# Kernel optimization log

Measured on AMD Instinct MI355X. Metric: run time of the kernel, lower is better.

Reference implementation:

```python
import jax, jax.numpy as jnp
import numpy as np

NUM_ITERS = 5
NUM_SPATIAL = 3          # S: xyz spatial dims
THETA_ALPHA = 1.0
THETA_BETA = 1.0
THETA_GAMMA = 8.0


def _gauss_filter(f, q):
    """Exact Gaussian filtering (math the permutohedral lattice pl.apply approximates).
    f: [D, N] features, q: [C, N] values.
    out[:, i] = sum_j exp(-0.5 * ||f_i - f_j||^2) * q[:, j]
    """
    f2 = jnp.sum(f * f, axis=0)                       # [N]
    d2 = f2[:, None] + f2[None, :] - 2.0 * (f.T @ f)  # [N, N] squared distances
    K = jnp.exp(-0.5 * d2)                            # symmetric Gaussian kernel
    return q @ K                                      # [C, N]


def setup_inputs() -> dict:
    key = jax.random.key(0)
    k1, k2 = jax.random.split(key)
    C, N, D = 10, 8192, 6
    unaries = jax.random.normal(k1, (C, N), dtype=jnp.float32)
    feat = jax.random.normal(k2, (D, N), dtype=jnp.float32)
    # learned params: diagonal init for filter weights, Potts (-I) compatibility
    spatial_weights = jnp.eye(C, dtype=jnp.float32)
    bilateral_weights = jnp.eye(C, dtype=jnp.float32)
    compatibility_matrix = -jnp.eye(C, dtype=jnp.float32)
    return {
        "unaries": unaries,
        "feat": feat,
        "spatial_weights": spatial_weights,
        "bilateral_weights": bilateral_weights,
        "compatibility_matrix": compatibility_matrix,
    }


def reference(unaries, feat, spatial_weights, bilateral_weights, compatibility_matrix):
    # Pre-scaled features (torch code scales per-iteration, but with
    # theta_alpha=theta_beta=1.0 the in-place aliasing division is a no-op).
    sp_feat = feat[:NUM_SPATIAL] / THETA_GAMMA                      # [S, N]
    bl_feat = jnp.concatenate(
        [feat[:NUM_SPATIAL] / THETA_ALPHA, feat[NUM_SPATIAL:] / THETA_BETA],
        axis=0,
    )                                                               # [S+F, N]

    q = unaries
    for _ in range(NUM_ITERS):
        p = jax.nn.softmax(q, axis=0)                               # over classes
        spatial_out = _gauss_filter(sp_feat, p)                     # [C, N]
        bilateral_out = _gauss_filter(bl_feat, p)                   # [C, N]
        message_passing = spatial_weights @ spatial_out + bilateral_weights @ bilateral_out
        pairwise = compatibility_matrix @ message_passing
        q = unaries - pairwise
    return q
```

## Files before the change

kernel.cpp:

```cpp
#include <hip/hip_runtime.h>
#include <math.h>

#define N 8192
#define C 10
#define NUM_ITERS 5
#define FBLOCK 1024
#define IBLK 32
#define NBLK (N / IBLK)
#define JW (N / 16)
#define NS (JW / 32)
#define LOG2E 1.44269504088896340736f
#define C3 (LOG2E / 64.0f)

typedef _Float16 half8 __attribute__((ext_vector_type(8)));
typedef _Float16 half4 __attribute__((ext_vector_type(4)));
typedef _Float16 half2 __attribute__((ext_vector_type(2)));
typedef float f32x4 __attribute__((ext_vector_type(4)));

#define WS_AJS 0
#define WS_AJB (N * 16)
#define WS_PF0 (N * 32)
#define WS_PF1 (N * 64)
#define PFIDX(n, c) ((((n) >> 4) * 16 + (c)) * 16 + ((n) & 15))

static __device__ __forceinline__ half4 expcvt(f32x4 d) {
    float e0 = __builtin_amdgcn_exp2f(d[0]);
    float e1 = __builtin_amdgcn_exp2f(d[1]);
    float e2 = __builtin_amdgcn_exp2f(d[2]);
    float e3 = __builtin_amdgcn_exp2f(d[3]);
    half2 lo = __builtin_bit_cast(half2, __builtin_amdgcn_cvt_pkrtz(e0, e1));
    half2 hi = __builtin_bit_cast(half2, __builtin_amdgcn_cvt_pkrtz(e2, e3));
    half4 r = {lo[0], lo[1], hi[0], hi[1]};
    return r;
}

#define GROUP(AF, PF_, B1A, B1B, ACCA, ACCB)                                         \
    {                                                                                \
        f32x4 _da = __builtin_amdgcn_mfma_f32_16x16x16f16(AF, B1A, zero, 0, 0, 0);   \
        f32x4 _db = __builtin_amdgcn_mfma_f32_16x16x16f16(AF, B1B, zero, 0, 0, 0);   \
        half4 _wa = expcvt(_da), _wb = expcvt(_db);                                  \
        ACCA = __builtin_amdgcn_mfma_f32_16x16x16f16(_wa, PF_, ACCA, 0, 0, 0);       \
        ACCB = __builtin_amdgcn_mfma_f32_16x16x16f16(_wb, PF_, ACCB, 0, 0, 0);       \
    }

__global__ __launch_bounds__(256) void init_kernel(
    const float* __restrict__ unaries, const float* __restrict__ feat,
    half8* __restrict__ ajs8, half8* __restrict__ ajb8,
    _Float16* __restrict__ pf0, _Float16* __restrict__ pf1) {
    int n = blockIdx.x * 256 + threadIdx.x;
    float f6[6];
#pragma unroll
    for (int d = 0; d < 6; ++d) f6[d] = feat[d * N + n];
    float h3 = 0.5f * (f6[0] * f6[0] + f6[1] * f6[1] + f6[2] * f6[2]);
    float h6v = h3 + 0.5f * (f6[3] * f6[3] + f6[4] * f6[4] + f6[5] * f6[5]);
    half8 a = {};
    a[0] = (_Float16)(f6[0] * C3);
    a[1] = (_Float16)(f6[1] * C3);
    a[2] = (_Float16)(f6[2] * C3);
    a[6] = (_Float16)(-h3 * C3);
    a[7] = (_Float16)1.0f;
    ajs8[n] = a;
    half8 b;
#pragma unroll
    for (int d = 0; d < 6; ++d) b[d] = (_Float16)(f6[d] * LOG2E);
    b[6] = (_Float16)(-h6v * LOG2E);
    b[7] = (_Float16)1.0f;
    ajb8[n] = b;

    float q[C];
#pragma unroll
    for (int c = 0; c < C; ++c) q[c] = unaries[c * N + n];
    float m = q[0];
#pragma unroll
    for (int c = 1; c < C; ++c) m = fmaxf(m, q[c]);
    float e[C], s = 0.0f;
#pragma unroll
    for (int c = 0; c < C; ++c) {
        e[c] = __builtin_amdgcn_exp2f((q[c] - m) * LOG2E);
        s += e[c];
    }
    float inv = 1.0f / s;
#pragma unroll
    for (int c = 0; c < C; ++c) pf0[PFIDX(n, c)] = (_Float16)(e[c] * inv);
#pragma unroll
    for (int c = C; c < 16; ++c) {
        pf0[PFIDX(n, c)] = (_Float16)0.0f;
        pf1[PFIDX(n, c)] = (_Float16)0.0f;
    }
}

__global__ __launch_bounds__(FBLOCK, 4) void fused_kernel(
    const float* __restrict__ unaries, const float* __restrict__ feat,
    const float* __restrict__ SW, const float* __restrict__ BW,
    const float* __restrict__ CM,
    const half4* __restrict__ ajs_g, const half4* __restrict__ ajb_g,
    const _Float16* __restrict__ pf_in, _Float16* __restrict__ pf_out,
    float* __restrict__ out, int is_last) {
    __shared__ float rbuf[16 * 1024];
    int t = threadIdx.x;
    int i0 = blockIdx.x * IBLK;
    int lane = t & 63;
    int w = t >> 6;
    int il = lane & 15;
    int quad = lane >> 4;
    int h = quad & 1;
    bool klo = (quad < 2);
    const half4 hz = {};
    const f32x4 zero = {0.f, 0.f, 0.f, 0.f};

    half4 b1s0, b1s1, b1b0, b1b1;
#pragma unroll
    for (int s = 0; s < 2; ++s) {
        int i = i0 + s * 16 + il;
        float g0 = feat[0 * N + i], g1 = feat[1 * N + i], g2 = feat[2 * N + i];
        float g3 = feat[3 * N + i], g4 = feat[4 * N + i], g5 = feat[5 * N + i];
        float h3 = 0.5f * (g0 * g0 + g1 * g1 + g2 * g2);
        float h6v = h3 + 0.5f * (g3 * g3 + g4 * g4 + g5 * g5);
        half4 slo = {(_Float16)g0, (_Float16)g1, (_Float16)g2, (_Float16)0.0f};
        half4 shi = {(_Float16)0.0f, (_Float16)0.0f, (_Float16)1.0f, (_Float16)(-h3 * C3)};
        half4 blo = {(_Float16)g0, (_Float16)g1, (_Float16)g2, (_Float16)g3};
        half4 bhi = {(_Float16)g4, (_Float16)g5, (_Float16)1.0f, (_Float16)(-h6v * LOG2E)};
        half4 vs = klo ? (h ? shi : slo) : hz;
        half4 vb = klo ? (h ? bhi : blo) : hz;
        if (s == 0) { b1s0 = vs; b1b0 = vb; } else { b1s1 = vs; b1b1 = vb; }
    }

    f32x4 as0 = zero, as1 = zero, ab0 = zero, ab1 = zero;

    int jw = w * JW;
    const half4* pfv = (const half4*)pf_in;

    half4 cvs0 = ajs_g[(jw + il) * 2 + h];
    half4 cvs1 = ajs_g[(jw + 16 + il) * 2 + h];
    half4 cvb0 = ajb_g[(jw + il) * 2 + h];
    half4 cvb1 = ajb_g[(jw + 16 + il) * 2 + h];
    half4 cp0 = pfv[((jw >> 4) * 16 + il) * 4 + quad];
    half4 cp1 = pfv[((jw >> 4) * 16 + 16 + il) * 4 + quad];

#pragma unroll 4
    for (int k = 0; k < NS; ++k) {
        int jn = jw + (((k + 1) & (NS - 1)) * 32);
        half4 nvs0 = ajs_g[(jn + il) * 2 + h];
        half4 nvs1 = ajs_g[(jn + 16 + il) * 2 + h];
        half4 nvb0 = ajb_g[(jn + il) * 2 + h];
        half4 nvb1 = ajb_g[(jn + 16 + il) * 2 + h];
        half4 np0 = pfv[((jn >> 4) * 16 + il) * 4 + quad];
        half4 np1 = pfv[((jn >> 4) * 16 + 16 + il) * 4 + quad];

        GROUP(cvs0, cp0, b1s0, b1s1, as0, as1);
        GROUP(cvs1, cp1, b1s0, b1s1, as0, as1);
        GROUP(cvb0, cp0, b1b0, b1b1, ab0, ab1);
        GROUP(cvb1, cp1, b1b0, b1b1, ab0, ab1);

        cvs0 = nvs0; cvs1 = nvs1; cvb0 = nvb0; cvb1 = nvb1;
        cp0 = np0; cp1 = np1;
    }

    {
        float* rb = rbuf + w * 1024;
#pragma unroll
        for (int r = 0; r < 4; ++r) {
            rb[r * 64 + lane]       = as0[r];
            rb[256 + r * 64 + lane] = as1[r];
            rb[512 + r * 64 + lane] = ab0[r];
            rb[768 + r * 64 + lane] = ab1[r];
        }
    }
    __syncthreads();
    {
        float tot = 0.f;
#pragma unroll
        for (int w2 = 0; w2 < 16; ++w2) tot += rbuf[w2 * 1024 + t];
        rbuf[t] = tot;
    }
    __syncthreads();

    if (t < IBLK) {
        int i = i0 + t;
        int sub = t >> 4, ql = (t & 15) >> 2, rr = t & 3;
        float sp[C], bl[C];
#pragma unroll
        for (int c = 0; c < C; ++c) {
            int base = sub * 256 + rr * 64 + ql * 16 + c;
            sp[c] = rbuf[base];
            bl[c] = rbuf[base + 512];
        }
        float msg[C];
#pragma unroll
        for (int c = 0; c < C; ++c) {
            float m = 0.f;
#pragma unroll
            for (int k = 0; k < C; ++k)
                m += SW[c * C + k] * sp[k] + BW[c * C + k] * bl[k];
            msg[c] = m;
        }
        float qq[C];
#pragma unroll
        for (int c = 0; c < C; ++c) {
            float pw = 0.f;
#pragma unroll
            for (int k = 0; k < C; ++k) pw += CM[c * C + k] * msg[k];
            qq[c] = unaries[c * N + i] - pw;
        }
        if (is_last) {
#pragma unroll
            for (int c = 0; c < C; ++c) out[c * N + i] = qq[c];
        } else {
            float m = qq[0];
#pragma unroll
            for (int c = 1; c < C; ++c) m = fmaxf(m, qq[c]);
            float e[C], s = 0.0f;
#pragma unroll
            for (int c = 0; c < C; ++c) {
                e[c] = __builtin_amdgcn_exp2f((qq[c] - m) * LOG2E);
                s += e[c];
            }
            float inv = 1.0f / s;
#pragma unroll
            for (int c = 0; c < C; ++c) pf_out[PFIDX(i, c)] = (_Float16)(e[c] * inv);
        }
    }
}

extern "C" void kernel_launch(void* const* d_in, const int* in_sizes, int n_in,
                              void* d_out, int out_size, void* d_ws, size_t ws_size,
                              hipStream_t stream) {
    const float* unaries = (const float*)d_in[0];
    const float* feat    = (const float*)d_in[1];
    const float* SW      = (const float*)d_in[2];
    const float* BW      = (const float*)d_in[3];
    const float* CM      = (const float*)d_in[4];
    float* out = (float*)d_out;

    char* ws = (char*)d_ws;
    half8* ajs    = (half8*)(ws + WS_AJS);
    half8* ajb    = (half8*)(ws + WS_AJB);
    _Float16* pf0 = (_Float16*)(ws + WS_PF0);
    _Float16* pf1 = (_Float16*)(ws + WS_PF1);

    init_kernel<<<N / 256, 256, 0, stream>>>(unaries, feat, ajs, ajb, pf0, pf1);
    const _Float16* pin = pf0;
    _Float16* pout = pf1;
    for (int it = 1; it <= NUM_ITERS; ++it) {
        fused_kernel<<<NBLK, FBLOCK, 0, stream>>>(
            unaries, feat, SW, BW, CM, (const half4*)ajs, (const half4*)ajb,
            pin, pout, out, it == NUM_ITERS ? 1 : 0);
        const _Float16* tmp = pout;
        pout = (_Float16*)pin;
        pin = tmp;
    }
}
```

Measured before the change: 167.2 us.

## Shrink row tile to 16 rows per block and drop software prefetch

Each block now computes 16 output rows instead of 32. That halves the per-wave accumulators and the per-block reduction buffer, and doubles the block count. The register-level double-buffered prefetch of the j-tile operands is removed and loads are issued inside the loop, with the occupancy hint raised from 4 to 8. The aim is more occupancy and a smaller LDS and register footprint. In exchange, each loaded A and P fragment is reused for one B column tile instead of two, which doubles global and L2 traffic per MFMA, and latency hiding now depends on occupancy rather than explicit prefetch.

After: 193.5 us. +15.7%, slower.

```diff
diff --git a/kernel.cpp b/kernel.cpp
--- a/kernel.cpp
+++ b/kernel.cpp
@@ -5,7 +5,7 @@
 #define C 10
 #define NUM_ITERS 5
 #define FBLOCK 1024
-#define IBLK 32
+#define IBLK 16
 #define NBLK (N / IBLK)
 #define JW (N / 16)
 #define NS (JW / 32)
@@ -34,13 +34,11 @@
     return r;
 }
 
-#define GROUP(AF, PF_, B1A, B1B, ACCA, ACCB)                                         \
+#define GROUP(AF, PF_, B1, ACC)                                                      \
     {                                                                                \
-        f32x4 _da = __builtin_amdgcn_mfma_f32_16x16x16f16(AF, B1A, zero, 0, 0, 0);   \
-        f32x4 _db = __builtin_amdgcn_mfma_f32_16x16x16f16(AF, B1B, zero, 0, 0, 0);   \
-        half4 _wa = expcvt(_da), _wb = expcvt(_db);                                  \
-        ACCA = __builtin_amdgcn_mfma_f32_16x16x16f16(_wa, PF_, ACCA, 0, 0, 0);       \
-        ACCB = __builtin_amdgcn_mfma_f32_16x16x16f16(_wb, PF_, ACCB, 0, 0, 0);       \
+        f32x4 _d = __builtin_amdgcn_mfma_f32_16x16x16f16(AF, B1, zero, 0, 0, 0);     \
+        half4 _w = expcvt(_d);                                                       \
+        ACC = __builtin_amdgcn_mfma_f32_16x16x16f16(_w, PF_, ACC, 0, 0, 0);          \
     }
 
 __global__ __launch_bounds__(256) void init_kernel(
@@ -89,14 +87,14 @@
     }
 }
 
-__global__ __launch_bounds__(FBLOCK, 4) void fused_kernel(
+__global__ __launch_bounds__(FBLOCK, 8) void fused_kernel(
     const float* __restrict__ unaries, const float* __restrict__ feat,
     const float* __restrict__ SW, const float* __restrict__ BW,
     const float* __restrict__ CM,
     const half4* __restrict__ ajs_g, const half4* __restrict__ ajb_g,
     const _Float16* __restrict__ pf_in, _Float16* __restrict__ pf_out,
     float* __restrict__ out, int is_last) {
-    __shared__ float rbuf[16 * 1024];
+    __shared__ float rbuf[16 * 512];
     int t = threadIdx.x;
     int i0 = blockIdx.x * IBLK;
     int lane = t & 63;
@@ -108,10 +106,9 @@
     const half4 hz = {};
     const f32x4 zero = {0.f, 0.f, 0.f, 0.f};
 
-    half4 b1s0, b1s1, b1b0, b1b1;
-#pragma unroll
-    for (int s = 0; s < 2; ++s) {
-        int i = i0 + s * 16 + il;
+    half4 b1s, b1b;
+    {
+        int i = i0 + il;
         float g0 = feat[0 * N + i], g1 = feat[1 * N + i], g2 = feat[2 * N + i];
         float g3 = feat[3 * N + i], g4 = feat[4 * N + i], g5 = feat[5 * N + i];
         float h3 = 0.5f * (g0 * g0 + g1 * g1 + g2 * g2);
@@ -120,78 +117,60 @@
         half4 shi = {(_Float16)0.0f, (_Float16)0.0f, (_Float16)1.0f, (_Float16)(-h3 * C3)};
         half4 blo = {(_Float16)g0, (_Float16)g1, (_Float16)g2, (_Float16)g3};
         half4 bhi = {(_Float16)g4, (_Float16)g5, (_Float16)1.0f, (_Float16)(-h6v * LOG2E)};
-        half4 vs = klo ? (h ? shi : slo) : hz;
-        half4 vb = klo ? (h ? bhi : blo) : hz;
-        if (s == 0) { b1s0 = vs; b1b0 = vb; } else { b1s1 = vs; b1b1 = vb; }
-    }
-
-    f32x4 as0 = zero, as1 = zero, ab0 = zero, ab1 = zero;
+        b1s = klo ? (h ? shi : slo) : hz;
+        b1b = klo ? (h ? bhi : blo) : hz;
+    }
+
+    f32x4 acc_s = zero, acc_b = zero;
 
     int jw = w * JW;
     const half4* pfv = (const half4*)pf_in;
 
-    half4 cvs0 = ajs_g[(jw + il) * 2 + h];
-    half4 cvs1 = ajs_g[(jw + 16 + il) * 2 + h];
-    half4 cvb0 = ajb_g[(jw + il) * 2 + h];
-    half4 cvb1 = ajb_g[(jw + 16 + il) * 2 + h];
-    half4 cp0 = pfv[((jw >> 4) * 16 + il) * 4 + quad];
-    half4 cp1 = pfv[((jw >> 4) * 16 + 16 + il) * 4 + quad];
-
-#pragma unroll 4
+#pragma unroll 2
     for (int k = 0; k < NS; ++k) {
-        int jn = jw + (((k + 1) & (NS - 1)) * 32);
-        half4 nvs0 = ajs_g[(jn + il) * 2 + h];
-        half4 nvs1 = ajs_g[(jn + 16 + il) * 2 + h];
-        half4 nvb0 = ajb_g[(jn + il) * 2 + h];
-        half4 nvb1 = ajb_g[(jn + 16 + il) * 2 + h];
-        half4 np0 = pfv[((jn >> 4) * 16 + il) * 4 + quad];
-        half4 np1 = pfv[((jn >> 4) * 16 + 16 + il) * 4 + quad];
-
-        GROUP(cvs0, cp0, b1s0, b1s1, as0, as1);
-        GROUP(cvs1, cp1, b1s0, b1s1, as0, as1);
-        GROUP(cvb0, cp0, b1b0, b1b1, ab0, ab1);
-        GROUP(cvb1, cp1, b1b0, b1b1, ab0, ab1);
-
-        cvs0 = nvs0; cvs1 = nvs1; cvb0 = nvb0; cvb1 = nvb1;
-        cp0 = np0; cp1 = np1;
+        int j0 = jw + k * 32;
+        half4 cvs0 = ajs_g[(j0 + il) * 2 + h];
+        half4 cvs1 = ajs_g[(j0 + 16 + il) * 2 + h];
+        half4 cvb0 = ajb_g[(j0 + il) * 2 + h];
+        half4 cvb1 = ajb_g[(j0 + 16 + il) * 2 + h];
+        half4 cp0 = pfv[((j0 >> 4) * 16 + il) * 4 + quad];
+        half4 cp1 = pfv[(((j0 >> 4) + 1) * 16 + il) * 4 + quad];
+
+        GROUP(cvs0, cp0, b1s, acc_s);
+        GROUP(cvs1, cp1, b1s, acc_s);
+        GROUP(cvb0, cp0, b1b, acc_b);
+        GROUP(cvb1, cp1, b1b, acc_b);
     }
 
     {
-        float* rb = rbuf + w * 1024;
+        float* rb = rbuf + w * 512;
 #pragma unroll
         for (int r = 0; r < 4; ++r) {
-            rb[r * 64 + lane]       = as0[r];
-            rb[256 + r * 64 + lane] = as1[r];
-            rb[512 + r * 64 + lane] = ab0[r];
-            rb[768 + r * 64 + lane] = ab1[r];
+            rb[r * 64 + lane]       = acc_s[r];
+            rb[256 + r * 64 + lane] = acc_b[r];
         }
     }
     __syncthreads();
-    {
+    if (t < 512) {
         float tot = 0.f;
 #pragma unroll
-        for (int w2 = 0; w2 < 16; ++w2) tot += rbuf[w2 * 1024 + t];
+        for (int w2 = 0; w2 < 16; ++w2) tot += rbuf[w2 * 512 + t];
         rbuf[t] = tot;
     }
     __syncthreads();
 
     if (t < IBLK) {
         int i = i0 + t;
-        int sub = t >> 4, ql = (t & 15) >> 2, rr = t & 3;
-        float sp[C], bl[C];
-#pragma unroll
-        for (int c = 0; c < C; ++c) {
-            int base = sub * 256 + rr * 64 + ql * 16 + c;
-            sp[c] = rbuf[base];
-            bl[c] = rbuf[base + 512];
-        }
+        int q16 = t >> 2, r = t & 3;
+        int base = r * 64 + q16 * 16;
         float msg[C];
 #pragma unroll
         for (int c = 0; c < C; ++c) {
             float m = 0.f;
 #pragma unroll
-            for (int k = 0; k < C; ++k)
-                m += SW[c * C + k] * sp[k] + BW[c * C + k] * bl[k];
+            for (int kk = 0; kk < C; ++kk)
+                m += SW[c * C + kk] * rbuf[base + kk] +
+                     BW[c * C + kk] * rbuf[256 + base + kk];
             msg[c] = m;
         }
         float qq[C];
@@ -199,7 +178,7 @@
         for (int c = 0; c < C; ++c) {
             float pw = 0.f;
 #pragma unroll
-            for (int k = 0; k < C; ++k) pw += CM[c * C + k] * msg[k];
+            for (int kk = 0; kk < C; ++kk) pw += CM[c * C + kk] * msg[kk];
             qq[c] = unaries[c * N + i] - pw;
         }
         if (is_last) {
```

## Software-pipeline distance MFMAs ahead of exp and accumulate MFMAs

Applied to the files above, without the earlier changes.

Restructures the inner j-loop into a two-stage software pipeline. The distance MFMAs for the next chunk are issued before the exp/convert and accumulation MFMAs of the current chunk, with double-buffered operand loads. This lets MFMA latency and transcendental VALU work overlap instead of each group waiting on its own distance result. It raises register pressure from holding eight f32x4 distance tiles plus two operand sets, and the fixed trip count of 7 hardcodes NS=16.

Result: no change. 166.1 us (-0.7%).

```diff
diff --git a/kernel.cpp b/kernel.cpp
--- a/kernel.cpp
+++ b/kernel.cpp
@@ -34,14 +34,8 @@
     return r;
 }
 
-#define GROUP(AF, PF_, B1A, B1B, ACCA, ACCB)                                         \
-    {                                                                                \
-        f32x4 _da = __builtin_amdgcn_mfma_f32_16x16x16f16(AF, B1A, zero, 0, 0, 0);   \
-        f32x4 _db = __builtin_amdgcn_mfma_f32_16x16x16f16(AF, B1B, zero, 0, 0, 0);   \
-        half4 _wa = expcvt(_da), _wb = expcvt(_db);                                  \
-        ACCA = __builtin_amdgcn_mfma_f32_16x16x16f16(_wa, PF_, ACCA, 0, 0, 0);       \
-        ACCB = __builtin_amdgcn_mfma_f32_16x16x16f16(_wb, PF_, ACCB, 0, 0, 0);       \
-    }
+struct Ops { half4 vs0, vs1, vb0, vb1, p0, p1; };
+struct Dset { f32x4 d0, d1, d2, d3, d4, d5, d6, d7; };
 
 __global__ __launch_bounds__(256) void init_kernel(
     const float* __restrict__ unaries, const float* __restrict__ feat,
@@ -126,35 +120,67 @@
     }
 
     f32x4 as0 = zero, as1 = zero, ab0 = zero, ab1 = zero;
-
     int jw = w * JW;
     const half4* pfv = (const half4*)pf_in;
 
-    half4 cvs0 = ajs_g[(jw + il) * 2 + h];
-    half4 cvs1 = ajs_g[(jw + 16 + il) * 2 + h];
-    half4 cvb0 = ajb_g[(jw + il) * 2 + h];
-    half4 cvb1 = ajb_g[(jw + 16 + il) * 2 + h];
-    half4 cp0 = pfv[((jw >> 4) * 16 + il) * 4 + quad];
-    half4 cp1 = pfv[((jw >> 4) * 16 + 16 + il) * 4 + quad];
-
-#pragma unroll 4
-    for (int k = 0; k < NS; ++k) {
-        int jn = jw + (((k + 1) & (NS - 1)) * 32);
-        half4 nvs0 = ajs_g[(jn + il) * 2 + h];
-        half4 nvs1 = ajs_g[(jn + 16 + il) * 2 + h];
-        half4 nvb0 = ajb_g[(jn + il) * 2 + h];
-        half4 nvb1 = ajb_g[(jn + 16 + il) * 2 + h];
-        half4 np0 = pfv[((jn >> 4) * 16 + il) * 4 + quad];
-        half4 np1 = pfv[((jn >> 4) * 16 + 16 + il) * 4 + quad];
-
-        GROUP(cvs0, cp0, b1s0, b1s1, as0, as1);
-        GROUP(cvs1, cp1, b1s0, b1s1, as0, as1);
-        GROUP(cvb0, cp0, b1b0, b1b1, ab0, ab1);
-        GROUP(cvb1, cp1, b1b0, b1b1, ab0, ab1);
-
-        cvs0 = nvs0; cvs1 = nvs1; cvb0 = nvb0; cvb1 = nvb1;
-        cp0 = np0; cp1 = np1;
-    }
+#define LOAD_OPS(O, K)                                                     \
+    {                                                                      \
+        int _j0 = jw + ((K) & (NS - 1)) * 32;                              \
+        O.vs0 = ajs_g[(_j0 + il) * 2 + h];                                 \
+        O.vs1 = ajs_g[(_j0 + 16 + il) * 2 + h];                            \
+        O.vb0 = ajb_g[(_j0 + il) * 2 + h];                                 \
+        O.vb1 = ajb_g[(_j0 + 16 + il) * 2 + h];                            \
+        O.p0 = pfv[((_j0 >> 4) * 16 + il) * 4 + quad];                     \
+        O.p1 = pfv[(((_j0 >> 4) + 1) * 16 + il) * 4 + quad];               \
+    }
+#define G1(D, O)                                                               \
+    {                                                                          \
+        D.d0 = __builtin_amdgcn_mfma_f32_16x16x16f16(O.vs0, b1s0, zero, 0, 0, 0); \
+        D.d1 = __builtin_amdgcn_mfma_f32_16x16x16f16(O.vs0, b1s1, zero, 0, 0, 0); \
+        D.d2 = __builtin_amdgcn_mfma_f32_16x16x16f16(O.vs1, b1s0, zero, 0, 0, 0); \
+        D.d3 = __builtin_amdgcn_mfma_f32_16x16x16f16(O.vs1, b1s1, zero, 0, 0, 0); \
+        D.d4 = __builtin_amdgcn_mfma_f32_16x16x16f16(O.vb0, b1b0, zero, 0, 0, 0); \
+        D.d5 = __builtin_amdgcn_mfma_f32_16x16x16f16(O.vb0, b1b1, zero, 0, 0, 0); \
+        D.d6 = __builtin_amdgcn_mfma_f32_16x16x16f16(O.vb1, b1b0, zero, 0, 0, 0); \
+        D.d7 = __builtin_amdgcn_mfma_f32_16x16x16f16(O.vb1, b1b1, zero, 0, 0, 0); \
+    }
+#define G2(D, O)                                                               \
+    {                                                                          \
+        half4 _w0 = expcvt(D.d0), _w1 = expcvt(D.d1);                          \
+        half4 _w2 = expcvt(D.d2), _w3 = expcvt(D.d3);                          \
+        half4 _w4 = expcvt(D.d4), _w5 = expcvt(D.d5);                          \
+        half4 _w6 = expcvt(D.d6), _w7 = expcvt(D.d7);                          \
+        as0 = __builtin_amdgcn_mfma_f32_16x16x16f16(_w0, O.p0, as0, 0, 0, 0);  \
+        as1 = __builtin_amdgcn_mfma_f32_16x16x16f16(_w1, O.p0, as1, 0, 0, 0);  \
+        as0 = __builtin_amdgcn_mfma_f32_16x16x16f16(_w2, O.p1, as0, 0, 0, 0);  \
+        as1 = __builtin_amdgcn_mfma_f32_16x16x16f16(_w3, O.p1, as1, 0, 0, 0);  \
+        ab0 = __builtin_amdgcn_mfma_f32_16x16x16f16(_w4, O.p0, ab0, 0, 0, 0);  \
+        ab1 = __builtin_amdgcn_mfma_f32_16x16x16f16(_w5, O.p0, ab1, 0, 0, 0);  \
+        ab0 = __builtin_amdgcn_mfma_f32_16x16x16f16(_w6, O.p1, ab0, 0, 0, 0);  \
+        ab1 = __builtin_amdgcn_mfma_f32_16x16x16f16(_w7, O.p1, ab1, 0, 0, 0);  \
+    }
+
+    Ops opA, opB;
+    Dset dd;
+    LOAD_OPS(opA, 0);
+    LOAD_OPS(opB, 1);
+    G1(dd, opA);
+
+    for (int m = 0; m < 7; ++m) {
+        G2(dd, opA);
+        LOAD_OPS(opA, 2 * m + 2);
+        G1(dd, opB);
+        G2(dd, opB);
+        LOAD_OPS(opB, 2 * m + 3);
+        G1(dd, opA);
+    }
+    G2(dd, opA);
+    G1(dd, opB);
+    G2(dd, opB);
+
+#undef LOAD_OPS
+#undef G1
+#undef G2
 
     {
         float* rb = rbuf + w * 1024;
```
